# Optimization experiments

Measured on AMD Instinct MI355X. Metric: run time of the kernel, lower is better.

The kernel has to match this reference:

```python
import jax, jax.numpy as jnp
import numpy as np
import math

B, L, DP, DB, H, DH = 1, 256, 128, 128, 8, 32


def _ln(x, g, b, eps=1e-5):
    m = x.mean(-1, keepdims=True)
    v = x.var(-1, keepdims=True)
    return (x - m) / jnp.sqrt(v + eps) * g + b


def setup_inputs() -> dict:
    key = jax.random.key(0)
    ks = jax.random.split(key, 12)
    s_in = 1.0 / math.sqrt(DP)
    s_hd = 1.0 / math.sqrt(H * DH)
    return {
        "pair": jax.random.normal(ks[0], (B, L, L, DP), jnp.float32),
        "bias": jax.random.normal(ks[1], (B, L, L, DB), jnp.float32),
        "mask": jax.random.randint(ks[2], (B, L), 0, 2, jnp.int32),
        "g_pair": jnp.ones((DP,), jnp.float32),
        "b_pair": jnp.zeros((DP,), jnp.float32),
        "g_bias": jnp.ones((DB,), jnp.float32),
        "b_bias": jnp.zeros((DB,), jnp.float32),
        "Wq": jax.random.normal(ks[3], (DP, H * DH), jnp.float32) * s_in,
        "Wk": jax.random.normal(ks[4], (DP, H * DH), jnp.float32) * s_in,
        "Wv": jax.random.normal(ks[5], (DP, H * DH), jnp.float32) * s_in,
        "Wb": jax.random.normal(ks[6], (DB, H), jnp.float32) * s_in,
        "Wg": jax.random.normal(ks[7], (DP, H * DH), jnp.float32) * s_in,
        "bg": jnp.ones((H * DH,), jnp.float32),
        "Wo": jax.random.normal(ks[8], (H * DH, DP), jnp.float32) * s_hd,
        "bo": jnp.zeros((DP,), jnp.float32),
    }


def reference(pair, bias, mask, g_pair, b_pair, g_bias, b_bias,
              Wq, Wk, Wv, Wb, Wg, bg, Wo, bo):
    is_row = True
    scaling = 1.0 / math.sqrt(DH)

    mask_b = (mask == 0)                               # [B,L], True = masked
    mask_2d = mask_b[:, None, :] | mask_b[:, :, None]  # [B,L,L]

    p = jnp.nan_to_num(pair)
    bi = jnp.nan_to_num(bias)
    if is_row:
        p = p.transpose(0, 2, 1, 3)
        bi = bi.transpose(0, 2, 1, 3)
        mask_2d = mask_2d.transpose(0, 2, 1)

    pn = _ln(p, g_pair, b_pair)        # [B,L,L,DP]
    bn = _ln(bi, g_bias, b_bias)       # [B,L,L,DB]

    q = (pn @ Wq).reshape(B, L, L, H, DH) * scaling
    k = (pn @ Wk).reshape(B, L, L, H, DH) / math.sqrt(L)
    v = (pn @ Wv).reshape(B, L, L, H, DH)
    b_proj = bn @ Wb                   # [B,L,L,H]
    gate = jax.nn.sigmoid(pn @ Wg + bg)  # [B,L,L,H*DH]

    # scores summed over the axial (n) axis AND head dim k
    attn = jnp.einsum('bnihk,bnjhk->bijh', q, k) + b_proj
    attn = jnp.where(mask_2d[..., None], -1e9, attn)
    attn = jax.nn.softmax(attn, axis=-2)  # over j

    out = jnp.einsum('bijh,bkjhd->bikhd', attn, v).reshape(B, L, L, H * DH)
    out = gate * out
    out = out @ Wo + bo                # [B,L,L,DP]
    if is_row:
        out = out.transpose(0, 2, 1, 3)
    # note: faithful to source — output mask uses the (permuted) mask_2d frame
    out = jnp.where(mask_2d[..., None], 0.0, out)
    return out
```

## Files before the change

kernel.cpp:

```cpp
#include <hip/hip_runtime.h>
#include <math.h>


typedef unsigned short u16;
typedef __attribute__((ext_vector_type(8))) short short8;
typedef __attribute__((ext_vector_type(4))) short short4v;
typedef __attribute__((ext_vector_type(4))) float float4v;

__device__ __forceinline__ u16 f2bf(float f) {
  unsigned int u = __float_as_uint(f);
  u += 0x7FFFu + ((u >> 16) & 1u);
  return (u16)(u >> 16);
}
__device__ __forceinline__ float bf2f(u16 h) {
  return __uint_as_float(((unsigned int)h) << 16);
}

__global__ __launch_bounds__(256) void k_ln(const float* __restrict__ x,
                                            const float* __restrict__ g,
                                            const float* __restrict__ b,
                                            u16* __restrict__ y) {
  int p = blockIdx.x * 4 + (threadIdx.x >> 6);
  int lane = threadIdx.x & 63;
  float2 xv = *(const float2*)(x + (size_t)p * 128 + lane * 2);
  float x0 = xv.x, x1 = xv.y;
  float s = x0 + x1, ss = x0 * x0 + x1 * x1;
#pragma unroll
  for (int off = 32; off; off >>= 1) {
    s += __shfl_xor(s, off);
    ss += __shfl_xor(ss, off);
  }
  float m = s * (1.0f / 128.0f);
  float v = ss * (1.0f / 128.0f) - m * m;
  float inv = rsqrtf(v + 1e-5f);
  float2 gv = *(const float2*)(g + lane * 2);
  float2 bv = *(const float2*)(b + lane * 2);
  float y0 = (x0 - m) * inv * gv.x + bv.x;
  float y1 = (x1 - m) * inv * gv.y + bv.y;
  unsigned int pk = (unsigned int)f2bf(y0) | ((unsigned int)f2bf(y1) << 16);
  *(unsigned int*)(y + (size_t)p * 128 + lane * 2) = pk;
}

__global__ __launch_bounds__(256) void k_lnbias_bproj(const float* __restrict__ x,
                                                      const float* __restrict__ g,
                                                      const float* __restrict__ b,
                                                      const float* __restrict__ Wb,
                                                      float* __restrict__ Bp) {
  const int t = threadIdx.x;
  const int row = t >> 3, h = t & 7;
  const int p = blockIdx.x * 32 + row;
  const int r = p >> 8, sc = p & 255;
  const float* rp = x + (size_t)p * 128 + h * 16;
  float4 xv[4];
#pragma unroll
  for (int i = 0; i < 4; ++i) xv[i] = ((const float4*)rp)[i];
  float s = 0.f, ss = 0.f;
#pragma unroll
  for (int i = 0; i < 4; ++i) {
    s += (xv[i].x + xv[i].y) + (xv[i].z + xv[i].w);
    ss += (xv[i].x * xv[i].x + xv[i].y * xv[i].y) + (xv[i].z * xv[i].z + xv[i].w * xv[i].w);
  }
#pragma unroll
  for (int off = 1; off <= 4; off <<= 1) {
    s += __shfl_xor(s, off);
    ss += __shfl_xor(ss, off);
  }
  float m = s * (1.0f / 128.0f);
  float var = ss * (1.0f / 128.0f) - m * m;
  float inv = rsqrtf(var + 1e-5f);
  float part[8];
#pragma unroll
  for (int hh = 0; hh < 8; ++hh) part[hh] = 0.f;
  const float4* g4 = (const float4*)(g + h * 16);
  const float4* b4 = (const float4*)(b + h * 16);
#pragma unroll
  for (int i4 = 0; i4 < 4; ++i4) {
    float4 gv = g4[i4], bv = b4[i4];
    float xs[4] = {xv[i4].x, xv[i4].y, xv[i4].z, xv[i4].w};
    float gs[4] = {gv.x, gv.y, gv.z, gv.w};
    float bs[4] = {bv.x, bv.y, bv.z, bv.w};
#pragma unroll
    for (int q = 0; q < 4; ++q) {
      int k = h * 16 + i4 * 4 + q;
      float xn = (xs[q] - m) * inv * gs[q] + bs[q];
      float4 w0 = *(const float4*)(Wb + k * 8);
      float4 w1 = *(const float4*)(Wb + k * 8 + 4);
      part[0] += xn * w0.x;
      part[1] += xn * w0.y;
      part[2] += xn * w0.z;
      part[3] += xn * w0.w;
      part[4] += xn * w1.x;
      part[5] += xn * w1.y;
      part[6] += xn * w1.z;
      part[7] += xn * w1.w;
    }
  }
#pragma unroll
  for (int off = 1; off <= 4; off <<= 1) {
#pragma unroll
    for (int hh = 0; hh < 8; ++hh) part[hh] += __shfl_xor(part[hh], off);
  }
  float val = (h == 0) ? part[0]
            : (h == 1) ? part[1]
            : (h == 2) ? part[2]
            : (h == 3) ? part[3]
            : (h == 4) ? part[4]
            : (h == 5) ? part[5]
            : (h == 6) ? part[6]
                       : part[7];
  Bp[(size_t)h * 65536 + (size_t)sc * 256 + r] = val;
}

__global__ __launch_bounds__(256) void k_wcvt(const float* __restrict__ Wq,
                                              const float* __restrict__ Wk,
                                              const float* __restrict__ Wv,
                                              const float* __restrict__ Wg,
                                              const float* __restrict__ Wo,
                                              u16* __restrict__ Wtb,
                                              u16* __restrict__ Wotb) {
  int idx = blockIdx.x * 256 + threadIdx.x;
  if (idx < 131072) {
    int w = idx >> 15, r = idx & 32767;
    int n = r >> 7, k = r & 127;
    const float* W = (w == 0) ? Wq : (w == 1) ? Wk : (w == 2) ? Wv : Wg;
    Wtb[(size_t)w * 32768 + n * 128 + k] = f2bf(W[k * 256 + n]);
  } else {
    int r = idx - 131072;
    int c = r >> 8, e = r & 255;
    Wotb[c * 256 + e] = f2bf(Wo[e * 128 + c]);
  }
}

__global__ __launch_bounds__(256) void k_proj_qkg(const u16* __restrict__ PNb,
                                                  const u16* __restrict__ Wtb,
                                                  const float* __restrict__ bg,
                                                  u16* __restrict__ Qr4,
                                                  u16* __restrict__ Kr4,
                                                  u16* __restrict__ G2) {
  const int t = threadIdx.x;
  const int wid = t >> 6, lane = t & 63;
  const int mrow = lane & 15, quad = lane >> 4;
  const int stripe = blockIdx.x;
  const int n0 = blockIdx.y * 64;
  const int wsel3 = blockIdx.z;
  const int wsel = (wsel3 == 2) ? 3 : wsel3;
  const u16* Wt = Wtb + (size_t)wsel * 32768;
  u16* dst = (wsel3 == 0) ? Qr4 : (wsel3 == 1) ? Kr4 : G2;

  short8 bfr[4][4];
#pragma unroll
  for (int nt = 0; nt < 4; ++nt)
#pragma unroll
    for (int kk = 0; kk < 4; ++kk)
      bfr[nt][kk] = *(const short8*)(Wt + (size_t)(n0 + nt * 16 + mrow) * 128 + kk * 32 + quad * 8);

  float bgv[4];
#pragma unroll
  for (int nt = 0; nt < 4; ++nt) bgv[nt] = bg[n0 + nt * 16 + mrow];

  for (int it = 0; it < 4; ++it) {
    const int pw = stripe * 512 + it * 128 + wid * 32;
    short8 afr[2][4];
#pragma unroll
    for (int mt = 0; mt < 2; ++mt)
#pragma unroll
      for (int kk = 0; kk < 4; ++kk)
        afr[mt][kk] =
            *(const short8*)(PNb + (size_t)(pw + mt * 16 + mrow) * 128 + kk * 32 + quad * 8);
    float4v acc[2][4];
#pragma unroll
    for (int mt = 0; mt < 2; ++mt)
#pragma unroll
      for (int nt = 0; nt < 4; ++nt) acc[mt][nt] = (float4v){0.f, 0.f, 0.f, 0.f};
#pragma unroll
    for (int kk = 0; kk < 4; ++kk)
#pragma unroll
      for (int mt = 0; mt < 2; ++mt)
#pragma unroll
        for (int nt = 0; nt < 4; ++nt)
          acc[mt][nt] = __builtin_amdgcn_mfma_f32_16x16x32_bf16(afr[mt][kk], bfr[nt][kk],
                                                                acc[mt][nt], 0, 0, 0);
#pragma unroll
    for (int mt = 0; mt < 2; ++mt) {
      const int prow4 = ((pw + mt * 16) >> 2) + quad;
#pragma unroll
      for (int nt = 0; nt < 4; ++nt) {
        const int n = n0 + nt * 16 + mrow;
        short4v pk;
#pragma unroll
        for (int reg = 0; reg < 4; ++reg) {
          float v = acc[mt][nt][reg];
          if (wsel3 == 0) v *= 0.17677669529663687f;
          else if (wsel3 == 1) v *= 0.0625f;
          else v = 1.f / (1.f + expf(-(v + bgv[nt])));
          pk[reg] = (short)f2bf(v);
        }
        *(short4v*)(dst + ((size_t)prow4 * 256 + n) * 4) = pk;
      }
    }
  }
}

__global__ __launch_bounds__(256) void k_projv(const u16* __restrict__ PNb,
                                               const u16* __restrict__ Wtb,
                                               u16* __restrict__ Vtb) {
  __shared__ u16 sb[128 * 136];
  const int t = threadIdx.x;
  const int wid = t >> 6, lane = t & 63;
  const int mrow = lane & 15, quad = lane >> 4;
  const int sc = blockIdx.x >> 1;
  const int r0 = (blockIdx.x & 1) * 128;
  short8 afr[2][4];
#pragma unroll
  for (int mt = 0; mt < 2; ++mt) {
    const int p = (r0 + wid * 32 + mt * 16 + mrow) * 256 + sc;
    const u16* ar = PNb + (size_t)p * 128 + quad * 8;
#pragma unroll
    for (int kk = 0; kk < 4; ++kk) afr[mt][kk] = *(const short8*)(ar + kk * 32);
  }
  const u16* Wt = Wtb + (size_t)2 * 32768;
  for (int half = 0; half < 2; ++half) {
#pragma unroll
    for (int nt8 = 0; nt8 < 8; ++nt8) {
      const int nt = half * 8 + nt8;
      float4v acc[2];
      acc[0] = (float4v){0.f, 0.f, 0.f, 0.f};
      acc[1] = (float4v){0.f, 0.f, 0.f, 0.f};
      const u16* br = Wt + (size_t)(nt * 16 + mrow) * 128 + quad * 8;
#pragma unroll
      for (int kk = 0; kk < 4; ++kk) {
        short8 bfr = *(const short8*)(br + kk * 32);
#pragma unroll
        for (int mt = 0; mt < 2; ++mt)
          acc[mt] = __builtin_amdgcn_mfma_f32_16x16x32_bf16(afr[mt][kk], bfr, acc[mt], 0, 0, 0);
      }
#pragma unroll
      for (int mt = 0; mt < 2; ++mt)
#pragma unroll
        for (int reg = 0; reg < 4; ++reg)
          sb[(wid * 32 + mt * 16 + quad * 4 + reg) * 136 + nt8 * 16 + mrow] =
              f2bf(acc[mt][reg]);
    }
    __syncthreads();
#pragma unroll
    for (int it = 0; it < 8; ++it) {
      int u = it * 256 + t;
      int c = u & 127, rg = u >> 7;
      short8 vv;
#pragma unroll
      for (int q = 0; q < 8; ++q) vv[q] = (short)sb[(rg * 8 + q) * 136 + c];
      int n = half * 128 + c;
      int h = n >> 5, d = n & 31;
      *(short8*)(Vtb + (size_t)h * 2097152 + (size_t)(sc * 32 + d) * 256 + r0 + rg * 8) = vv;
    }
    __syncthreads();
  }
}

__global__ __launch_bounds__(256) void k_logits_mfma(const u16* __restrict__ Qr4,
                                                     const u16* __restrict__ Kr4,
                                                     float* __restrict__ Lg2) {
  __shared__ u16 Qs[128 * 72];
  __shared__ u16 Ks[128 * 72];
  const int t = threadIdx.x;
  const int wid = t >> 6, lane = t & 63;
  const int mrow = lane & 15, quad = lane >> 4;
  const int i0 = (blockIdx.x >> 1) * 128, j0 = (blockIdx.x & 1) * 128;
  const int h = blockIdx.y;
  const int z = blockIdx.z;
  const int wi = wid >> 1, wj = wid & 1;
  float4v acc[4][4];
#pragma unroll
  for (int a = 0; a < 4; ++a)
#pragma unroll
    for (int bq = 0; bq < 4; ++bq) acc[a][bq] = (float4v){0.f, 0.f, 0.f, 0.f};

  for (int g = 0; g < 4; ++g) {
    const int sc4 = z * 4 + g;
    for (int sub = 0; sub < 2; ++sub) {
      __syncthreads();
#pragma unroll
      for (int itq = 0; itq < 4; ++itq) {
        int u = itq * 256 + t;
        int i_loc = u >> 3, c16 = sub * 8 + (u & 7);
        size_t qoff = ((size_t)((i0 + i_loc) * 64 + sc4) * 256 + h * 32 + c16 * 2) * 4;
        *(short8*)&Qs[i_loc * 72 + (u & 7) * 8] = *(const short8*)(Qr4 + qoff);
        size_t koff = ((size_t)((j0 + i_loc) * 64 + sc4) * 256 + h * 32 + c16 * 2) * 4;
        *(short8*)&Ks[i_loc * 72 + (u & 7) * 8] = *(const short8*)(Kr4 + koff);
      }
      __syncthreads();
#pragma unroll
      for (int kk = 0; kk < 2; ++kk) {
        short8 afr[4], bfr[4];
#pragma unroll
        for (int mt = 0; mt < 4; ++mt)
          afr[mt] = *(const short8*)&Qs[(wi * 64 + mt * 16 + mrow) * 72 + kk * 32 + quad * 8];
#pragma unroll
        for (int nn = 0; nn < 4; ++nn)
          bfr[nn] = *(const short8*)&Ks[(wj * 64 + nn * 16 + mrow) * 72 + kk * 32 + quad * 8];
#pragma unroll
        for (int mt = 0; mt < 4; ++mt)
#pragma unroll
          for (int nn = 0; nn < 4; ++nn)
            acc[mt][nn] =
                __builtin_amdgcn_mfma_f32_16x16x32_bf16(afr[mt], bfr[nn], acc[mt][nn], 0, 0, 0);
      }
    }
  }
  float* slab = Lg2 + ((size_t)z * 8 + h) * 65536;
#pragma unroll
  for (int mt = 0; mt < 4; ++mt)
#pragma unroll
    for (int nn = 0; nn < 4; ++nn) {
      int j = j0 + wj * 64 + nn * 16 + mrow;
#pragma unroll
      for (int reg = 0; reg < 4; ++reg) {
        int i = i0 + wi * 64 + mt * 16 + quad * 4 + reg;
        slab[(size_t)i * 256 + j] = acc[mt][nn][reg];
      }
    }
}

__global__ __launch_bounds__(256) void k_softmax(const float* __restrict__ Bp,
                                                 const float* __restrict__ Lg2,
                                                 const int* __restrict__ mask,
                                                 u16* __restrict__ Ab) {
  const int i = blockIdx.x, h = blockIdx.y;
  const int j = threadIdx.x;
  __shared__ float red[4], red2[4];
  const size_t off = (size_t)h * 65536 + (size_t)i * 256 + j;
  float x = Bp[off];
#pragma unroll
  for (int z = 0; z < 16; ++z) x += Lg2[(size_t)z * 524288 + off];
  bool mi = (mask[i] == 0);
  if (mi || (mask[j] == 0)) x = -1e9f;
  float mx = x;
#pragma unroll
  for (int off2 = 32; off2; off2 >>= 1) mx = fmaxf(mx, __shfl_xor(mx, off2));
  int wave = j >> 6;
  if ((j & 63) == 0) red[wave] = mx;
  __syncthreads();
  mx = fmaxf(fmaxf(red[0], red[1]), fmaxf(red[2], red[3]));
  float e = expf(x - mx);
  float sm = e;
#pragma unroll
  for (int off2 = 32; off2; off2 >>= 1) sm += __shfl_xor(sm, off2);
  if ((j & 63) == 0) red2[wave] = sm;
  __syncthreads();
  sm = red2[0] + red2[1] + red2[2] + red2[3];
  Ab[off] = f2bf(e / sm);
}

__global__ __launch_bounds__(256) void k_av_mfma(const u16* __restrict__ Ab,
                                                 const u16* __restrict__ Vtb,
                                                 const u16* __restrict__ G2,
                                                 u16* __restrict__ GOb) {
  __shared__ u16 As[64 * 264];
  const int t = threadIdx.x;
  const int wid = t >> 6, lane = t & 63;
  const int mrow = lane & 15, quad = lane >> 4;
  const int h = blockIdx.z;
  const int i0 = blockIdx.y * 64;
  const u16* ag = Ab + (size_t)h * 65536 + (size_t)i0 * 256;
#pragma unroll
  for (int u = 0; u < 8; ++u) {
    int id = u * 256 + t;
    int rr = id >> 5, c8 = (id & 31) * 8;
    *(short8*)&As[rr * 264 + c8] = *(const short8*)(ag + (size_t)rr * 256 + c8);
  }
  __syncthreads();
  const u16* vg = Vtb + (size_t)h * 2097152;
  for (int nt4 = 0; nt4 < 4; ++nt4) {
    const int nbase = blockIdx.x * 1024 + wid * 256 + nt4 * 64;
    float4v acc[4][4];
#pragma unroll
    for (int a = 0; a < 4; ++a)
#pragma unroll
      for (int bq = 0; bq < 4; ++bq) acc[a][bq] = (float4v){0.f, 0.f, 0.f, 0.f};
#pragma unroll
    for (int kk = 0; kk < 8; ++kk) {
      short8 afr[4], bfr[4];
#pragma unroll
      for (int mt = 0; mt < 4; ++mt)
        afr[mt] = *(const short8*)&As[(mt * 16 + mrow) * 264 + kk * 32 + quad * 8];
#pragma unroll
      for (int nn = 0; nn < 4; ++nn)
        bfr[nn] = *(const short8*)(vg + (size_t)(nbase + nn * 16 + mrow) * 256 + kk * 32 + quad * 8);
#pragma unroll
      for (int mt = 0; mt < 4; ++mt)
#pragma unroll
        for (int nn = 0; nn < 4; ++nn)
          acc[mt][nn] = __builtin_amdgcn_mfma_f32_16x16x32_bf16(afr[mt], bfr[nn], acc[mt][nn], 0, 0, 0);
    }
#pragma unroll
    for (int mt = 0; mt < 4; ++mt)
#pragma unroll
      for (int nn = 0; nn < 4; ++nn) {
        const int kslot = (nbase + nn * 16) >> 5;
        const int d = (nn & 1) * 16 + mrow;
        const int e = h * 32 + d;
        const int p4 = kslot * 64 + ((i0 + mt * 16) >> 2) + quad;
        short4v g4 = *(const short4v*)(G2 + ((size_t)p4 * 256 + e) * 4);
#pragma unroll
        for (int reg = 0; reg < 4; ++reg) {
          int i = i0 + mt * 16 + quad * 4 + reg;
          size_t idx = ((size_t)i * 256 + kslot) * 256 + e;
          float gv = bf2f((u16)g4[reg]);
          GOb[idx] = f2bf(acc[mt][nn][reg] * gv);
        }
      }
  }
}

__global__ __launch_bounds__(256) void k_out_mfma(const u16* __restrict__ GOb,
                                                  const u16* __restrict__ Wotb,
                                                  const float* __restrict__ bo,
                                                  const int* __restrict__ mask,
                                                  float* __restrict__ out) {
  const int wid = threadIdx.x >> 6, lane = threadIdx.x & 63;
  const int mrow = lane & 15, quad = lane >> 4;
  const int m0 = blockIdx.x * 128 + wid * 32;
  short8 afr[2][8];
#pragma unroll
  for (int mt = 0; mt < 2; ++mt) {
    const u16* ar = GOb + (size_t)(m0 + mt * 16 + mrow) * 256 + quad * 8;
#pragma unroll
    for (int kk = 0; kk < 8; ++kk) afr[mt][kk] = *(const short8*)(ar + kk * 32);
  }
  for (int nt = 0; nt < 8; ++nt) {
    float4v acc[2];
    acc[0] = (float4v){0.f, 0.f, 0.f, 0.f};
    acc[1] = (float4v){0.f, 0.f, 0.f, 0.f};
    const u16* br = Wotb + (size_t)(nt * 16 + mrow) * 256 + quad * 8;
#pragma unroll
    for (int kk = 0; kk < 8; ++kk) {
      short8 bfr = *(const short8*)(br + kk * 32);
#pragma unroll
      for (int mt = 0; mt < 2; ++mt)
        acc[mt] = __builtin_amdgcn_mfma_f32_16x16x32_bf16(afr[mt][kk], bfr, acc[mt], 0, 0, 0);
    }
    const int c = nt * 16 + mrow;
    float bov = bo[c];
#pragma unroll
    for (int mt = 0; mt < 2; ++mt) {
#pragma unroll
      for (int reg = 0; reg < 4; ++reg) {
        int m = m0 + mt * 16 + quad * 4 + reg;
        int i = m >> 8, kq = m & 255;
        float v = acc[mt][reg] + bov;
        bool z = (mask[i] == 0) || (mask[kq] == 0);
        out[((size_t)kq * 256 + i) * 128 + c] = z ? 0.f : v;
      }
    }
  }
}

extern "C" void kernel_launch(void* const* d_in, const int* in_sizes, int n_in,
                              void* d_out, int out_size, void* d_ws, size_t ws_size,
                              hipStream_t stream) {
  const float* pair = (const float*)d_in[0];
  const float* bias = (const float*)d_in[1];
  const int* mask = (const int*)d_in[2];
  const float* g_pair = (const float*)d_in[3];
  const float* b_pair = (const float*)d_in[4];
  const float* g_bias = (const float*)d_in[5];
  const float* b_bias = (const float*)d_in[6];
  const float* Wq = (const float*)d_in[7];
  const float* Wk = (const float*)d_in[8];
  const float* Wv = (const float*)d_in[9];
  const float* Wb = (const float*)d_in[10];
  const float* Wg = (const float*)d_in[11];
  const float* bg = (const float*)d_in[12];
  const float* Wo = (const float*)d_in[13];
  const float* bo = (const float*)d_in[14];
  float* out = (float*)d_out;
  char* ws = (char*)d_ws;

  u16* PNb = (u16*)(ws + 0);
  u16* Qr4 = (u16*)(ws + 16777216);
  u16* Kr4 = (u16*)(ws + 50331648);
  u16* Vtb = (u16*)(ws + 83886080);
  u16* G2 = (u16*)(ws + 117440512);
  u16* GOb = (u16*)(ws + 150994944);
  float* Bp = (float*)(ws + 184549376);
  u16* Ab = (u16*)(ws + 186646528);
  u16* Wtb = (u16*)(ws + 187695104);
  u16* Wotb = (u16*)(ws + 187957248);
  float* Lg2 = (float*)(ws + 188022784);

  k_ln<<<16384, 256, 0, stream>>>(pair, g_pair, b_pair, PNb);
  k_wcvt<<<640, 256, 0, stream>>>(Wq, Wk, Wv, Wg, Wo, Wtb, Wotb);
  k_lnbias_bproj<<<2048, 256, 0, stream>>>(bias, g_bias, b_bias, Wb, Bp);
  k_proj_qkg<<<dim3(128, 4, 3), 256, 0, stream>>>(PNb, Wtb, bg, Qr4, Kr4, G2);
  k_projv<<<512, 256, 0, stream>>>(PNb, Wtb, Vtb);
  k_logits_mfma<<<dim3(4, 8, 16), 256, 0, stream>>>(Qr4, Kr4, Lg2);
  k_softmax<<<dim3(256, 8), 256, 0, stream>>>(Bp, Lg2, mask, Ab);
  k_av_mfma<<<dim3(8, 4, 8), 256, 0, stream>>>(Ab, Vtb, G2, GOb);
  k_out_mfma<<<512, 256, 0, stream>>>(GOb, Wotb, bo, mask, out);
}
```

Measured before the change: 338.2 us.

## Restructure V projection to keep weights in registers and drop LDS transpose

The V projection kernel now loads a 64-column slice of the weight into registers once and loops over row tiles, mirroring the QKG projection. It writes short4 results straight to the transposed V layout, which removes the shared-memory transpose and its barriers. The grid changes from 512 to 256x4 blocks. The direct stores are narrower and more scattered than the old 16-byte LDS-staged stores, so write coalescing may be worse. An unroll-2 pragma is also added to the QKG row loop.

```diff
diff --git a/kernel.cpp b/kernel.cpp
--- a/kernel.cpp
+++ b/kernel.cpp
@@ -158,6 +158,7 @@
 #pragma unroll
   for (int nt = 0; nt < 4; ++nt) bgv[nt] = bg[n0 + nt * 16 + mrow];
 
+#pragma unroll 2
   for (int it = 0; it < 4; ++it) {
     const int pw = stripe * 512 + it * 128 + wid * 32;
     short8 afr[2][4];
@@ -204,56 +205,56 @@
 __global__ __launch_bounds__(256) void k_projv(const u16* __restrict__ PNb,
                                                const u16* __restrict__ Wtb,
                                                u16* __restrict__ Vtb) {
-  __shared__ u16 sb[128 * 136];
   const int t = threadIdx.x;
   const int wid = t >> 6, lane = t & 63;
   const int mrow = lane & 15, quad = lane >> 4;
-  const int sc = blockIdx.x >> 1;
-  const int r0 = (blockIdx.x & 1) * 128;
-  short8 afr[2][4];
-#pragma unroll
-  for (int mt = 0; mt < 2; ++mt) {
-    const int p = (r0 + wid * 32 + mt * 16 + mrow) * 256 + sc;
-    const u16* ar = PNb + (size_t)p * 128 + quad * 8;
-#pragma unroll
-    for (int kk = 0; kk < 4; ++kk) afr[mt][kk] = *(const short8*)(ar + kk * 32);
-  }
+  const int sc = blockIdx.x;
+  const int n0 = blockIdx.y * 64;
   const u16* Wt = Wtb + (size_t)2 * 32768;
-  for (int half = 0; half < 2; ++half) {
-#pragma unroll
-    for (int nt8 = 0; nt8 < 8; ++nt8) {
-      const int nt = half * 8 + nt8;
-      float4v acc[2];
-      acc[0] = (float4v){0.f, 0.f, 0.f, 0.f};
-      acc[1] = (float4v){0.f, 0.f, 0.f, 0.f};
-      const u16* br = Wt + (size_t)(nt * 16 + mrow) * 128 + quad * 8;
-#pragma unroll
-      for (int kk = 0; kk < 4; ++kk) {
-        short8 bfr = *(const short8*)(br + kk * 32);
-#pragma unroll
-        for (int mt = 0; mt < 2; ++mt)
-          acc[mt] = __builtin_amdgcn_mfma_f32_16x16x32_bf16(afr[mt][kk], bfr, acc[mt], 0, 0, 0);
-      }
+
+  short8 bfr[4][4];
+#pragma unroll
+  for (int nt = 0; nt < 4; ++nt)
+#pragma unroll
+    for (int kk = 0; kk < 4; ++kk)
+      bfr[nt][kk] = *(const short8*)(Wt + (size_t)(n0 + nt * 16 + mrow) * 128 + kk * 32 + quad * 8);
+
+#pragma unroll 2
+  for (int it = 0; it < 2; ++it) {
+    const int rbase = it * 128 + wid * 32;
+    short8 afr[2][4];
+#pragma unroll
+    for (int mt = 0; mt < 2; ++mt)
+#pragma unroll
+      for (int kk = 0; kk < 4; ++kk)
+        afr[mt][kk] = *(const short8*)(PNb + ((size_t)(rbase + mt * 16 + mrow) * 256 + sc) * 128 +
+                                       kk * 32 + quad * 8);
+    float4v acc[2][4];
+#pragma unroll
+    for (int mt = 0; mt < 2; ++mt)
+#pragma unroll
+      for (int nt = 0; nt < 4; ++nt) acc[mt][nt] = (float4v){0.f, 0.f, 0.f, 0.f};
+#pragma unroll
+    for (int kk = 0; kk < 4; ++kk)
 #pragma unroll
       for (int mt = 0; mt < 2; ++mt)
 #pragma unroll
-        for (int reg = 0; reg < 4; ++reg)
-          sb[(wid * 32 + mt * 16 + quad * 4 + reg) * 136 + nt8 * 16 + mrow] =
-              f2bf(acc[mt][reg]);
-    }
-    __syncthreads();
-#pragma unroll
-    for (int it = 0; it < 8; ++it) {
-      int u = it * 256 + t;
-      int c = u & 127, rg = u >> 7;
-      short8 vv;
-#pragma unroll
-      for (int q = 0; q < 8; ++q) vv[q] = (short)sb[(rg * 8 + q) * 136 + c];
-      int n = half * 128 + c;
-      int h = n >> 5, d = n & 31;
-      *(short8*)(Vtb + (size_t)h * 2097152 + (size_t)(sc * 32 + d) * 256 + r0 + rg * 8) = vv;
-    }
-    __syncthreads();
+        for (int nt = 0; nt < 4; ++nt)
+          acc[mt][nt] = __builtin_amdgcn_mfma_f32_16x16x32_bf16(afr[mt][kk], bfr[nt][kk],
+                                                                acc[mt][nt], 0, 0, 0);
+#pragma unroll
+    for (int mt = 0; mt < 2; ++mt) {
+      const int j0 = rbase + mt * 16 + quad * 4;
+#pragma unroll
+      for (int nt = 0; nt < 4; ++nt) {
+        const int n = n0 + nt * 16 + mrow;
+        const int h = n >> 5, d = n & 31;
+        short4v pk;
+#pragma unroll
+        for (int reg = 0; reg < 4; ++reg) pk[reg] = (short)f2bf(acc[mt][nt][reg]);
+        *(short4v*)(Vtb + (size_t)h * 2097152 + (size_t)(sc * 32 + d) * 256 + j0) = pk;
+      }
+    }
   }
 }
 
@@ -492,7 +493,7 @@
   k_wcvt<<<640, 256, 0, stream>>>(Wq, Wk, Wv, Wg, Wo, Wtb, Wotb);
   k_lnbias_bproj<<<2048, 256, 0, stream>>>(bias, g_bias, b_bias, Wb, Bp);
   k_proj_qkg<<<dim3(128, 4, 3), 256, 0, stream>>>(PNb, Wtb, bg, Qr4, Kr4, G2);
-  k_projv<<<512, 256, 0, stream>>>(PNb, Wtb, Vtb);
+  k_projv<<<dim3(256, 4), 256, 0, stream>>>(PNb, Wtb, Vtb);
   k_logits_mfma<<<dim3(4, 8, 16), 256, 0, stream>>>(Qr4, Kr4, Lg2);
   k_softmax<<<dim3(256, 8), 256, 0, stream>>>(Bp, Lg2, mask, Ab);
   k_av_mfma<<<dim3(8, 4, 8), 256, 0, stream>>>(Ab, Vtb, G2, GOb);
```

Measured after the change: 331.7 us. About the same (-1.9%).
